# Optimization experiments

Measured on AMD Instinct MI355X. Metric: run time of the kernel, lower is better.

The kernel has to match this reference:

```python
import jax, jax.numpy as jnp
import numpy as np

B, T, D, BOT = 4, 4096, 2048, 256


def setup_inputs() -> dict:
    key = jax.random.key(0)
    k1, k2, k3, k4 = jax.random.split(key, 4)
    return {
        "hdc_chars": jax.random.normal(k1, (B, T, D), dtype=jnp.float32),
        "decay_matrix": jax.random.uniform(k2, (B, T, T), dtype=jnp.float32),
        "Wq": jax.random.normal(k3, (BOT, D), dtype=jnp.float32) * (D ** -0.5),
        "bq": jnp.zeros((BOT,), dtype=jnp.float32),
        "Wk": jax.random.normal(k4, (BOT, D), dtype=jnp.float32) * (D ** -0.5),
        "bk": jnp.zeros((BOT,), dtype=jnp.float32),
    }


def reference(hdc_chars, decay_matrix, Wq, bq, Wk, bk):
    # hdc_chars: [B,T,D]; decay_matrix: [B,T,T]
    bot = Wq.shape[0]
    scale = bot ** -0.5
    q = hdc_chars @ Wq.T + bq          # [B,T,bot]
    k = hdc_chars @ Wk.T + bk          # [B,T,bot]
    scores = jnp.einsum("btc,bsc->bts", q, k) * scale  # [B,T,T]
    t = scores.shape[-1]
    i = jnp.arange(t)[:, None]
    j = jnp.arange(t)[None, :]
    allowed = j <= i - 4               # tril(diagonal=-4): blocks local echo
    scores = jnp.where(allowed, scores, jnp.float32(-65000.0))
    resonance = jax.nn.softmax(scores, axis=-1)
    combined = 0.7 * decay_matrix + 0.3 * resonance
    return combined @ hdc_chars        # [B,T,D]
```

## Files before the change

kernel.cpp:

```cpp
#include <hip/hip_runtime.h>
#include <hip/hip_bf16.h>

#define BB 4
#define TT 4096
#define DD 2048
#define BOTC 256

typedef __bf16 bf16;
typedef __attribute__((ext_vector_type(4))) __bf16 bf16x4;
typedef __attribute__((ext_vector_type(8))) __bf16 bf16x8;
typedef __attribute__((ext_vector_type(4))) float f32x4;

constexpr int BM = 128, BN = 128, BK = 64;

__device__ __forceinline__ void async16(const void* g, bf16* l) {
  __builtin_amdgcn_global_load_lds((const __attribute__((address_space(1))) void*)g,
                                   (__attribute__((address_space(3))) void*)l, 16, 0, 0);
}

template <int EPI>
__global__ __launch_bounds__(256) void gemm_bt(
    const bf16* __restrict__ A, const bf16* __restrict__ Bm, void* __restrict__ Cout,
    const float* __restrict__ bias, int M, int N, int K, int ldA, int ldB,
    long sAb, long sBb, long sCb, float scale) {
  const int b = blockIdx.z;
  const int m0 = blockIdx.y * BM;
  const int n0 = blockIdx.x * BN;
  const int tid = threadIdx.x;
  const int lane = tid & 63;
  const int w = tid >> 6;
  const int wm = (w >> 1) * 64;
  const int wn = (w & 1) * 64;

  if (EPI == 2 && n0 > m0) return;

  __shared__ bf16 As[BM * BK];
  __shared__ bf16 Bs[BN * BK];

  f32x4 acc[4][4] = {};

  const bf16* Arow = A + (size_t)b * sAb + (size_t)m0 * ldA;
  const bf16* Brow = Bm + (size_t)b * sBb + (size_t)n0 * ldB;

  for (int k0 = 0; k0 < K; k0 += BK) {
#pragma unroll
    for (int j = 0; j < 4; ++j) {
      int c = j * 256 + tid;
      int row = c >> 3, kc = c & 7;
      int gk = kc ^ (row & 7);
      async16(Arow + (size_t)row * ldA + k0 + gk * 8, As + (size_t)c * 8);
      async16(Brow + (size_t)row * ldB + k0 + gk * 8, Bs + (size_t)c * 8);
    }
    __syncthreads();
    bf16x8 af[4][2], bfr[4][2];
#pragma unroll
    for (int mi = 0; mi < 4; ++mi)
#pragma unroll
      for (int kk = 0; kk < 2; ++kk) {
        int row = wm + mi * 16 + (lane & 15);
        int kc = kk * 4 + (lane >> 4);
        af[mi][kk] = *(const bf16x8*)(As + ((size_t)row * 8 + (kc ^ (row & 7))) * 8);
      }
#pragma unroll
    for (int ni = 0; ni < 4; ++ni)
#pragma unroll
      for (int kk = 0; kk < 2; ++kk) {
        int row = wn + ni * 16 + (lane & 15);
        int kc = kk * 4 + (lane >> 4);
        bfr[ni][kk] = *(const bf16x8*)(Bs + ((size_t)row * 8 + (kc ^ (row & 7))) * 8);
      }
#pragma unroll
    for (int kk = 0; kk < 2; ++kk)
#pragma unroll
      for (int mi = 0; mi < 4; ++mi)
#pragma unroll
        for (int ni = 0; ni < 4; ++ni)
          acc[mi][ni] = __builtin_amdgcn_mfma_f32_16x16x32_bf16(af[mi][kk], bfr[ni][kk], acc[mi][ni], 0, 0, 0);
    __syncthreads();
  }

  const int lcol = lane & 15;
  const int lrow = (lane >> 4) * 4;

  if (EPI == 0) {
    float* C = (float*)Cout + (size_t)b * sCb;
#pragma unroll
    for (int mi = 0; mi < 4; ++mi) {
      int rbase = m0 + wm + mi * 16 + lrow;
#pragma unroll
      for (int ni = 0; ni < 4; ++ni) {
        int col = n0 + wn + ni * 16 + lcol;
#pragma unroll
        for (int r = 0; r < 4; ++r)
          C[(size_t)(rbase + r) * N + col] = acc[mi][ni][r];
      }
    }
  } else if (EPI == 1) {
    bf16* C = (bf16*)Cout + (size_t)b * sCb;
#pragma unroll
    for (int mi = 0; mi < 4; ++mi) {
      int rbase = m0 + wm + mi * 16 + lrow;
#pragma unroll
      for (int ni = 0; ni < 4; ++ni) {
        int col = n0 + wn + ni * 16 + lcol;
        float bv = bias[col];
#pragma unroll
        for (int r = 0; r < 4; ++r)
          C[(size_t)(rbase + r) * N + col] = (bf16)(acc[mi][ni][r] + bv);
      }
    }
  } else {
    bf16* C = (bf16*)Cout + (size_t)b * sCb;
#pragma unroll
    for (int mi = 0; mi < 4; ++mi) {
      int rbase = m0 + wm + mi * 16 + lrow;
#pragma unroll
      for (int ni = 0; ni < 4; ++ni) {
        int col = n0 + wn + ni * 16 + lcol;
#pragma unroll
        for (int r = 0; r < 4; ++r) {
          int i = rbase + r;
          float v = acc[mi][ni][r] * scale;
          if (col > i - 4) v = -65000.0f;
          C[(size_t)i * N + col] = (bf16)v;
        }
      }
    }
  }
}

__global__ __launch_bounds__(256) void conv_transpose(
    const float* __restrict__ hdc, bf16* __restrict__ hb, bf16* __restrict__ hT) {
  __shared__ float tile[64][65];
  int b = blockIdx.z;
  int d0 = blockIdx.x * 64, t0 = blockIdx.y * 64;
  int tid = threadIdx.x;
  const float* src = hdc + (size_t)b * TT * DD;
  bf16* dstb = hb + (size_t)b * TT * DD;
  bf16* dstT = hT + (size_t)b * DD * TT;
  int c4 = tid & 15, r0 = tid >> 4;
#pragma unroll
  for (int rr = 0; rr < 4; ++rr) {
    int r = rr * 16 + r0;
    float4 v = *(const float4*)(src + (size_t)(t0 + r) * DD + d0 + c4 * 4);
    tile[r][c4 * 4 + 0] = v.x;
    tile[r][c4 * 4 + 1] = v.y;
    tile[r][c4 * 4 + 2] = v.z;
    tile[r][c4 * 4 + 3] = v.w;
    bf16x4 o;
    o[0] = (bf16)v.x; o[1] = (bf16)v.y; o[2] = (bf16)v.z; o[3] = (bf16)v.w;
    *(bf16x4*)(dstb + (size_t)(t0 + r) * DD + d0 + c4 * 4) = o;
  }
  __syncthreads();
  int tc = tid & 7, dr0 = tid >> 3;
#pragma unroll
  for (int rr = 0; rr < 2; ++rr) {
    int dr = rr * 32 + dr0;
    bf16x8 o;
#pragma unroll
    for (int e = 0; e < 8; ++e) o[e] = (bf16)tile[tc * 8 + e][dr];
    *(bf16x8*)(dstT + (size_t)(d0 + dr) * TT + t0 + tc * 8) = o;
  }
}

__global__ __launch_bounds__(256) void conv_w(
    const float* __restrict__ Wq, const float* __restrict__ Wk,
    const float* __restrict__ bq, const float* __restrict__ bk,
    bf16* __restrict__ Wqkb, float* __restrict__ bqk) {
  int i = blockIdx.x * 256 + threadIdx.x;
  float4 q = *(const float4*)(Wq + (size_t)i * 4);
  float4 k = *(const float4*)(Wk + (size_t)i * 4);
  bf16x4 qo, ko;
  qo[0] = (bf16)q.x; qo[1] = (bf16)q.y; qo[2] = (bf16)q.z; qo[3] = (bf16)q.w;
  ko[0] = (bf16)k.x; ko[1] = (bf16)k.y; ko[2] = (bf16)k.z; ko[3] = (bf16)k.w;
  *(bf16x4*)(Wqkb + (size_t)i * 4) = qo;
  *(bf16x4*)(Wqkb + (size_t)BOTC * DD + (size_t)i * 4) = ko;
  if (blockIdx.x == 0) {
    bqk[threadIdx.x] = bq[threadIdx.x];
    bqk[256 + threadIdx.x] = bk[threadIdx.x];
  }
}

__global__ __launch_bounds__(256) void softmax_combine(
    bf16* __restrict__ S, const float* __restrict__ decay) {
  int b = blockIdx.y, i = blockIdx.x;
  bf16* srow = S + ((size_t)b * TT + i) * TT;
  const float* drow = decay + ((size_t)b * TT + i) * TT;
  int t = threadIdx.x;
  int lane = t & 63, w = t >> 6;
  const int valid = i - 3;
  const int nc = valid > 0 ? (valid + 7) >> 3 : 0;

  float p[2][8];
  float inv = 0.f, pc = 0.f;

  if (valid > 0) {
    float s[2][8];
#pragma unroll
    for (int u = 0; u < 2; ++u) {
      int c = u * 256 + t;
      if (c < nc) {
        bf16x8 sv = *(const bf16x8*)(srow + (size_t)c * 8);
#pragma unroll
        for (int e = 0; e < 8; ++e) {
          int j = c * 8 + e;
          s[u][e] = j < valid ? (float)sv[e] : -INFINITY;
        }
      } else {
#pragma unroll
        for (int e = 0; e < 8; ++e) s[u][e] = -INFINITY;
      }
    }
    float m = s[0][0];
#pragma unroll
    for (int u = 0; u < 2; ++u)
#pragma unroll
      for (int e = 0; e < 8; ++e) m = fmaxf(m, s[u][e]);
#pragma unroll
    for (int off = 32; off > 0; off >>= 1) m = fmaxf(m, __shfl_xor(m, off));
    __shared__ float redm[4], reds[4];
    if (lane == 0) redm[w] = m;
    __syncthreads();
    m = fmaxf(fmaxf(redm[0], redm[1]), fmaxf(redm[2], redm[3]));

    float sum = 0.f;
#pragma unroll
    for (int u = 0; u < 2; ++u)
#pragma unroll
      for (int e = 0; e < 8; ++e) {
        p[u][e] = __expf(s[u][e] - m);
        sum += p[u][e];
      }
#pragma unroll
    for (int off = 32; off > 0; off >>= 1) sum += __shfl_xor(sum, off);
    if (lane == 0) reds[w] = sum;
    __syncthreads();
    sum = reds[0] + reds[1] + reds[2] + reds[3];
    inv = 0.3f / sum;
  } else {
    pc = 0.3f / 4096.0f;
#pragma unroll
    for (int u = 0; u < 2; ++u)
#pragma unroll
      for (int e = 0; e < 8; ++e) p[u][e] = 0.f;
  }

#pragma unroll
  for (int u = 0; u < 2; ++u) {
    int c = u * 256 + t;
    const float4* d4 = (const float4*)(drow + (size_t)c * 8);
    float4 da = d4[0], db = d4[1];
    float pv[8];
#pragma unroll
    for (int e = 0; e < 8; ++e) pv[e] = p[u][e] * inv + pc;
    bf16x8 o;
    o[0] = (bf16)(0.7f * da.x + pv[0]);
    o[1] = (bf16)(0.7f * da.y + pv[1]);
    o[2] = (bf16)(0.7f * da.z + pv[2]);
    o[3] = (bf16)(0.7f * da.w + pv[3]);
    o[4] = (bf16)(0.7f * db.x + pv[4]);
    o[5] = (bf16)(0.7f * db.y + pv[5]);
    o[6] = (bf16)(0.7f * db.z + pv[6]);
    o[7] = (bf16)(0.7f * db.w + pv[7]);
    *(bf16x8*)(srow + (size_t)c * 8) = o;
  }
}

extern "C" void kernel_launch(void* const* d_in, const int* in_sizes, int n_in,
                              void* d_out, int out_size, void* d_ws, size_t ws_size,
                              hipStream_t stream) {
  (void)in_sizes; (void)n_in; (void)out_size; (void)ws_size;
  const float* hdc = (const float*)d_in[0];
  const float* decay = (const float*)d_in[1];
  const float* Wq = (const float*)d_in[2];
  const float* bq = (const float*)d_in[3];
  const float* Wk = (const float*)d_in[4];
  const float* bk = (const float*)d_in[5];
  float* out = (float*)d_out;

  char* ws = (char*)d_ws;
  bf16* hdc_b = (bf16*)ws; ws += (size_t)BB * TT * DD * 2;
  bf16* hdcT  = (bf16*)ws; ws += (size_t)BB * TT * DD * 2;
  bf16* Wqkb  = (bf16*)ws; ws += (size_t)2 * BOTC * DD * 2;
  float* bqk  = (float*)ws; ws += 2 * BOTC * 4;
  bf16* qk    = (bf16*)ws; ws += (size_t)BB * TT * 2 * BOTC * 2;
  bf16* S     = (bf16*)ws; ws += (size_t)BB * TT * TT * 2;

  conv_transpose<<<dim3(DD / 64, TT / 64, BB), 256, 0, stream>>>(hdc, hdc_b, hdcT);
  conv_w<<<dim3(BOTC * DD / 1024), 256, 0, stream>>>(Wq, Wk, bq, bk, Wqkb, bqk);

  gemm_bt<1><<<dim3((2 * BOTC) / BN, (BB * TT) / BM, 1), 256, 0, stream>>>(
      hdc_b, Wqkb, qk, bqk, BB * TT, 2 * BOTC, DD, DD, DD, 0, 0, 0, 1.0f);

  gemm_bt<2><<<dim3(TT / BN, TT / BM, BB), 256, 0, stream>>>(
      qk, qk + BOTC, S, nullptr, TT, TT, BOTC, 2 * BOTC, 2 * BOTC,
      (long)TT * 2 * BOTC, (long)TT * 2 * BOTC, (long)TT * TT, 0.0625f);

  softmax_combine<<<dim3(TT, BB), 256, 0, stream>>>(S, decay);

  gemm_bt<0><<<dim3(DD / BN, TT / BM, BB), 256, 0, stream>>>(
      S, hdcT, out, nullptr, TT, DD, TT, TT, TT,
      (long)TT * TT, (long)DD * TT, (long)TT * DD, 1.0f);
}
```

Baseline: 975.0 us.

## Replace final GEMM with 256x256 tiled, 8-wave software-pipelined kernel

The combined-by-hdc GEMM now uses a dedicated 256x256-tile kernel with 512 threads. It double-buffers LDS in half-tiles and interleaves async global->LDS loads with MFMA quads, using explicit s_barrier, waitcnt and setprio scheduling. The aim is higher MFMA utilization and more data reuse per tile than the 128x128 generic kernel. In exchange it uses much more LDS and registers, and relies on hand-tuned waitcnt counts that must match the issued load count.

```diff
diff --git a/kernel.cpp b/kernel.cpp
--- a/kernel.cpp
+++ b/kernel.cpp
@@ -17,6 +17,11 @@
   __builtin_amdgcn_global_load_lds((const __attribute__((address_space(1))) void*)g,
                                    (__attribute__((address_space(3))) void*)l, 16, 0, 0);
 }
+
+#define SBAR asm volatile("s_barrier" ::: "memory")
+#define WAIT_LGKM0 asm volatile("s_waitcnt lgkmcnt(0)" ::: "memory")
+#define WAIT_VM6 asm volatile("s_waitcnt vmcnt(6)" ::: "memory")
+#define WAIT_VM0 asm volatile("s_waitcnt vmcnt(0)" ::: "memory")
 
 template <int EPI>
 __global__ __launch_bounds__(256) void gemm_bt(
@@ -82,20 +87,7 @@
   const int lcol = lane & 15;
   const int lrow = (lane >> 4) * 4;
 
-  if (EPI == 0) {
-    float* C = (float*)Cout + (size_t)b * sCb;
-#pragma unroll
-    for (int mi = 0; mi < 4; ++mi) {
-      int rbase = m0 + wm + mi * 16 + lrow;
-#pragma unroll
-      for (int ni = 0; ni < 4; ++ni) {
-        int col = n0 + wn + ni * 16 + lcol;
-#pragma unroll
-        for (int r = 0; r < 4; ++r)
-          C[(size_t)(rbase + r) * N + col] = acc[mi][ni][r];
-      }
-    }
-  } else if (EPI == 1) {
+  if (EPI == 1) {
     bf16* C = (bf16*)Cout + (size_t)b * sCb;
 #pragma unroll
     for (int mi = 0; mi < 4; ++mi) {
@@ -125,6 +117,154 @@
           C[(size_t)i * N + col] = (bf16)v;
         }
       }
+    }
+  }
+}
+
+__device__ __forceinline__ void stage_half(const bf16* __restrict__ src, int ld,
+                                           bf16* lds, int tid) {
+#pragma unroll
+  for (int j = 0; j < 2; ++j) {
+    int c = j * 512 + tid;
+    int row = c >> 3;
+    int gk = (c & 7) ^ (row & 7);
+    async16(src + (size_t)row * ld + gk * 8, lds + (size_t)c * 8);
+  }
+}
+
+__device__ __forceinline__ bf16x8 fragrd(const bf16* base, int lr, int kc) {
+  return *(const bf16x8*)(base + ((size_t)lr * 8 + (kc ^ (lr & 7))) * 8);
+}
+
+__device__ __forceinline__ void load_b4(const bf16* base, int wn, int fr, int fq,
+                                        bf16x8 (&bf_)[4][2]) {
+#pragma unroll
+  for (int ni = 0; ni < 4; ++ni)
+#pragma unroll
+    for (int kk = 0; kk < 2; ++kk)
+      bf_[ni][kk] = fragrd(base, (wn & 1) * 64 + ni * 16 + fr, kk * 4 + fq);
+}
+
+__device__ __forceinline__ void load_a4(const bf16* base, int qm, int fr, int fq,
+                                        bf16x8 (&a)[4][2]) {
+#pragma unroll
+  for (int mi = 0; mi < 4; ++mi)
+#pragma unroll
+    for (int kk = 0; kk < 2; ++kk)
+      a[mi][kk] = fragrd(base, qm * 64 + mi * 16 + fr, kk * 4 + fq);
+}
+
+__device__ __forceinline__ void mfma_quad(f32x4 (&acc)[8][4], const bf16x8 (&a)[4][2],
+                                          const bf16x8 (&bf_)[4][2], int qm, int qn) {
+  __builtin_amdgcn_s_setprio(1);
+#pragma unroll
+  for (int kk = 0; kk < 2; ++kk)
+#pragma unroll
+    for (int mi = 0; mi < 4; ++mi)
+#pragma unroll
+      for (int ni = 0; ni < 2; ++ni)
+        acc[qm * 4 + mi][qn * 2 + ni] = __builtin_amdgcn_mfma_f32_16x16x32_bf16(
+            a[mi][kk], bf_[qn * 2 + ni][kk], acc[qm * 4 + mi][qn * 2 + ni], 0, 0, 0);
+  __builtin_amdgcn_s_setprio(0);
+}
+
+__global__ __launch_bounds__(512, 2) void gemm256(
+    const bf16* __restrict__ A, const bf16* __restrict__ Bm, float* __restrict__ C,
+    int N, int K, int ldA, int ldB, long sAb, long sBb, long sCb) {
+  const int b = blockIdx.z;
+  const int m0 = blockIdx.y * 256;
+  const int n0 = blockIdx.x * 256;
+  const int tid = threadIdx.x;
+  const int lane = tid & 63;
+  const int w = tid >> 6;
+  const int wm = w >> 2;
+  const int wn = w & 3;
+  const int fr = lane & 15;
+  const int fq = lane >> 4;
+  const int bh = wn >> 1;
+  const int NKT = K >> 6;
+  const int NI = K >> 7;
+
+  __shared__ bf16 sA[2][2][8192];
+  __shared__ bf16 sB[2][2][8192];
+
+  const bf16* Ab = A + (size_t)b * sAb + (size_t)m0 * ldA;
+  const bf16* Bb = Bm + (size_t)b * sBb + (size_t)n0 * ldB;
+
+  f32x4 acc[8][4] = {};
+  bf16x8 a[4][2], bf_[4][2];
+
+  stage_half(Bb, ldB, &sB[0][0][0], tid);
+  stage_half(Bb + (size_t)128 * ldB, ldB, &sB[0][1][0], tid);
+  stage_half(Ab, ldA, &sA[0][0][0], tid);
+  stage_half(Ab + (size_t)128 * ldA, ldA, &sA[0][1][0], tid);
+  stage_half(Bb + 64, ldB, &sB[1][0][0], tid);
+  stage_half(Bb + (size_t)128 * ldB + 64, ldB, &sB[1][1][0], tid);
+  stage_half(Ab + 64, ldA, &sA[1][0][0], tid);
+  WAIT_VM6;
+  SBAR;
+
+  for (int i = 0; i < NI; ++i) {
+    const size_t kA1 = (size_t)(2 * i + 1) * 64;
+    int t2 = 2 * i + 2; if (t2 > NKT - 1) t2 = NKT - 1;
+    int t3 = 2 * i + 3; if (t3 > NKT - 1) t3 = NKT - 1;
+    const size_t k2 = (size_t)t2 * 64, k3 = (size_t)t3 * 64;
+
+    load_b4(&sB[0][bh][0], wn, fr, fq, bf_);
+    load_a4(&sA[0][wm][0], 0, fr, fq, a);
+    stage_half(Ab + (size_t)128 * ldA + kA1, ldA, &sA[1][1][0], tid);
+    SBAR; WAIT_LGKM0; __builtin_amdgcn_sched_barrier(0);
+    mfma_quad(acc, a, bf_, 0, 0);
+    SBAR;
+    stage_half(Bb + k2, ldB, &sB[0][0][0], tid);
+    SBAR;
+    mfma_quad(acc, a, bf_, 0, 1);
+    SBAR;
+    load_a4(&sA[0][wm][0], 1, fr, fq, a);
+    stage_half(Bb + (size_t)128 * ldB + k2, ldB, &sB[0][1][0], tid);
+    SBAR; WAIT_LGKM0; __builtin_amdgcn_sched_barrier(0);
+    mfma_quad(acc, a, bf_, 1, 0);
+    SBAR;
+    stage_half(Ab + k2, ldA, &sA[0][0][0], tid);
+    SBAR;
+    mfma_quad(acc, a, bf_, 1, 1);
+    WAIT_VM6;
+    SBAR;
+    load_b4(&sB[1][bh][0], wn, fr, fq, bf_);
+    load_a4(&sA[1][wm][0], 0, fr, fq, a);
+    stage_half(Ab + (size_t)128 * ldA + k2, ldA, &sA[0][1][0], tid);
+    SBAR; WAIT_LGKM0; __builtin_amdgcn_sched_barrier(0);
+    mfma_quad(acc, a, bf_, 0, 0);
+    SBAR;
+    stage_half(Bb + k3, ldB, &sB[1][0][0], tid);
+    SBAR;
+    mfma_quad(acc, a, bf_, 0, 1);
+    SBAR;
+    load_a4(&sA[1][wm][0], 1, fr, fq, a);
+    stage_half(Bb + (size_t)128 * ldB + k3, ldB, &sB[1][1][0], tid);
+    SBAR; WAIT_LGKM0; __builtin_amdgcn_sched_barrier(0);
+    mfma_quad(acc, a, bf_, 1, 0);
+    SBAR;
+    stage_half(Ab + k3, ldA, &sA[1][0][0], tid);
+    SBAR;
+    mfma_quad(acc, a, bf_, 1, 1);
+    WAIT_VM6;
+    SBAR;
+  }
+
+  WAIT_VM0;
+
+  float* Cb = C + (size_t)b * sCb;
+  const int lrow = fq * 4;
+#pragma unroll
+  for (int mi = 0; mi < 8; ++mi) {
+    int rbase = m0 + wm * 128 + mi * 16 + lrow;
+#pragma unroll
+    for (int ni = 0; ni < 4; ++ni) {
+      int col = n0 + wn * 64 + ni * 16 + fr;
+#pragma unroll
+      for (int r = 0; r < 4; ++r)
+        Cb[(size_t)(rbase + r) * N + col] = acc[mi][ni][r];
     }
   }
 }
@@ -298,7 +438,7 @@
 
   softmax_combine<<<dim3(TT, BB), 256, 0, stream>>>(S, decay);
 
-  gemm_bt<0><<<dim3(DD / BN, TT / BM, BB), 256, 0, stream>>>(
-      S, hdcT, out, nullptr, TT, DD, TT, TT, TT,
-      (long)TT * TT, (long)DD * TT, (long)TT * DD, 1.0f);
-}
+  gemm256<<<dim3(DD / 256, TT / 256, BB), 512, 0, stream>>>(
+      S, hdcT, out, DD, TT, TT, TT,
+      (long)TT * TT, (long)DD * TT, (long)TT * DD);
+}
```

New measurement: 906.4 us. 7.0% less time.
